# Performance work log

Measured on AMD Instinct MI355X. Metric: run time of the kernel, lower is better.

Reference implementation:

```python
import jax, jax.numpy as jnp
import numpy as np

N_NODES = 100000
N_EDGES = 1200000
IN_DIM, HIDDEN, OUT_DIM = 128, 64, 64


def setup_inputs() -> dict:
    key = jax.random.key(0)
    k1, k2, k3, k4 = jax.random.split(key, 4)
    x = jax.random.normal(k1, (N_NODES, IN_DIM), dtype=jnp.float32)
    edge_index = jax.random.randint(k2, (2, N_EDGES), 0, N_NODES, dtype=jnp.int64)
    # Glorot-style init for GCNConv linear weights (PyG uses glorot), zero bias.
    W1 = jax.random.normal(k3, (IN_DIM, HIDDEN), dtype=jnp.float32) * np.float32(np.sqrt(2.0 / (IN_DIM + HIDDEN)))
    b1 = jnp.zeros((HIDDEN,), dtype=jnp.float32)
    W2 = jax.random.normal(k4, (HIDDEN, OUT_DIM), dtype=jnp.float32) * np.float32(np.sqrt(2.0 / (HIDDEN + OUT_DIM)))
    b2 = jnp.zeros((OUT_DIM,), dtype=jnp.float32)
    return {"x": x, "edge_index": edge_index, "W1": W1, "b1": b1, "W2": W2, "b2": b2}


def _gcn_conv(h, src, dst, deg_inv_sqrt, W, b):
    # PyG GCNConv: out = scatter_add( norm * (h @ W)[src] -> dst ) + b
    n = h.shape[0]
    norm = deg_inv_sqrt[src] * deg_inv_sqrt[dst]            # [E+N]
    hw = h @ W                                              # [N, F_out]
    msg = hw[src] * norm[:, None]                           # [E+N, F_out] gather
    out = jnp.zeros((n, W.shape[1]), h.dtype).at[dst].add(msg)  # scatter-add
    return out + b


def reference(x, edge_index, W1, b1, W2, b2):
    n = x.shape[0]
    # Add self-loops (GCNConv default add_self_loops=True).
    loop = jnp.arange(n, dtype=edge_index.dtype)
    src = jnp.concatenate([edge_index[0], loop])  # source nodes
    dst = jnp.concatenate([edge_index[1], loop])  # target nodes (aggregation)
    # Symmetric normalization D^{-1/2} (A+I) D^{-1/2}; degree at targets.
    deg = jnp.zeros((n,), x.dtype).at[dst].add(jnp.ones((), x.dtype))
    deg_inv_sqrt = jnp.where(deg > 0, jax.lax.rsqrt(deg), 0.0)
    h = _gcn_conv(x, src, dst, deg_inv_sqrt, W1, b1)
    h = jax.nn.relu(h)
    h = _gcn_conv(h, src, dst, deg_inv_sqrt, W2, b2)
    h = jax.nn.relu(h)
    return h
```

## Files before the change

### kernel.cpp

```cpp
#include <hip/hip_runtime.h>
#include <hip/hip_fp16.h>
#include <cstdint>
#include <cstddef>

#define NN 100000
#define NE 1200000
#define NBKT 1563
#define CAP_B 1536
#define PBLK 256
#define PCHK ((NE + PBLK - 1) / PBLK)

typedef _Float16 f16x8 __attribute__((ext_vector_type(8)));
typedef float f32x4 __attribute__((ext_vector_type(4)));

__global__ void zero_kernel(int* __restrict__ cur, unsigned* __restrict__ ovfn) {
    int i = blockIdx.x * blockDim.x + threadIdx.x;
    if (i < NBKT) cur[i] = 0;
    if (i == NBKT) *ovfn = 0;
}

__global__ __launch_bounds__(256) void partition_hier(
    const int* __restrict__ ei, int* __restrict__ cur,
    unsigned* __restrict__ recs, unsigned* __restrict__ ovfn,
    uint2* __restrict__ ovf, int E) {
    __shared__ int hist[NBKT];
    __shared__ int base[NBKT];
    const int tid = threadIdx.x;
    for (int i = tid; i < NBKT; i += 256) hist[i] = 0;
    __syncthreads();
    const int lo = blockIdx.x * PCHK, hi = min(lo + PCHK, E);
    for (int e = lo + tid; e < hi; e += 256)
        atomicAdd(&hist[ei[E + e] >> 6], 1);
    __syncthreads();
    for (int i = tid; i < NBKT; i += 256) {
        int c = hist[i];
        base[i] = c ? atomicAdd(&cur[i], c) : 0;
        hist[i] = 0;
    }
    __syncthreads();
    for (int e = lo + tid; e < hi; e += 256) {
        int d = ei[E + e];
        int s = ei[e];
        int b = d >> 6;
        int lp = atomicAdd(&hist[b], 1);
        int pos = base[b] + lp;
        if (pos < CAP_B)
            recs[(size_t)b * CAP_B + pos] = ((unsigned)s << 6) | (unsigned)(d & 63);
        else {
            unsigned o = atomicAdd(ovfn, 1);
            if (o < 4096) ovf[o] = make_uint2((unsigned)s, (unsigned)d);
        }
    }
}

__global__ __launch_bounds__(256) void sort_bucket(
    const int* __restrict__ cur, unsigned* __restrict__ recs,
    const unsigned* __restrict__ ovfn, const uint2* __restrict__ ovf,
    float* __restrict__ dis, int* __restrict__ offn, int n) {
    __shared__ unsigned raw[CAP_B], srt[CAP_B];
    __shared__ int cnt[64], pfx[64], woff[64];
    const int b = blockIdx.x, tid = threadIdx.x;
    if (tid < 64) cnt[tid] = 0;
    const int c = min(cur[b], CAP_B);
    unsigned* slab = recs + (size_t)b * CAP_B;
    for (int i = tid; i < c; i += 256) raw[i] = slab[i];
    __syncthreads();
    for (int i = tid; i < c; i += 256) atomicAdd(&cnt[raw[i] & 63], 1);
    __syncthreads();
    if (tid < 64) pfx[tid] = cnt[tid];
    __syncthreads();
    for (int s = 1; s < 64; s <<= 1) {
        int v = (tid < 64 && tid >= s) ? pfx[tid - s] : 0;
        __syncthreads();
        if (tid < 64) pfx[tid] += v;
        __syncthreads();
    }
    if (tid < 64) woff[tid] = pfx[tid] - cnt[tid];
    __syncthreads();
    for (int i = tid; i < c; i += 256) {
        unsigned k = raw[i];
        int p = atomicAdd(&woff[k & 63], 1);
        srt[p] = k >> 6;
    }
    __syncthreads();
    for (int i = tid; i < c; i += 256) slab[i] = srt[i];
    if (tid < 64) {
        int g = b * 64 + tid;
        if (g < n) {
            int cc = cnt[tid];
            unsigned no = *ovfn;
            for (unsigned i = 0; i < no; i++)
                if ((int)ovf[i].y == g) cc++;
            dis[g] = rsqrtf((float)cc + 1.0f);
            offn[g] = pfx[tid] - cnt[tid];
        }
    }
}

template <bool HALF_OUT>
__global__ __launch_bounds__(256) void agg_bucket4(
    const int* __restrict__ cur, const unsigned* __restrict__ recs,
    const int* __restrict__ offn, const __half* __restrict__ hw,
    const float* __restrict__ dis, const float* __restrict__ bias,
    void* __restrict__ outv,
    const unsigned* __restrict__ ovfn, const uint2* __restrict__ ovf, int n) {
    __shared__ unsigned srec[CAP_B];
    __shared__ int soff[65];
    __shared__ float disD[64];
    const int b = blockIdx.x, tid = threadIdx.x;
    const int c = min(cur[b], CAP_B);
    const unsigned* slab = recs + (size_t)b * CAP_B;
    for (int i = tid; i < c; i += 256) srec[i] = slab[i];
    if (tid < 64) {
        int g = b * 64 + tid;
        disD[tid] = (g < n) ? dis[g] : 0.f;
        soff[tid] = (g < n) ? offn[g] : c;
    }
    if (tid == 0) soff[64] = c;
    __syncthreads();

    const uint2* hwq = (const uint2*)hw;
    const int slot = tid >> 4, sub = tid & 15;
    const unsigned no = *ovfn;
    const float4 bb = ((const float4*)bias)[sub];

#define LD1(q) { float2 g01 = __half22float2(*(__half2*)&(q).x); \
                 float2 g23 = __half22float2(*(__half2*)&(q).y); \
                 a0 += g01.x; a1 += g01.y; a2 += g23.x; a3 += g23.y; }

    for (int j = 0; j < 4; j++) {
        int nl = slot * 4 + j;
        int g = b * 64 + nl;
        if (g >= n) break;
        uint2 qs = hwq[(size_t)g * 16 + sub];
        float a0 = 0.f, a1 = 0.f, a2 = 0.f, a3 = 0.f;
        LD1(qs);

        int e = soff[nl], end = (nl < 63) ? soff[nl + 1] : soff[64];
        for (; e + 8 <= end; e += 8) {
            uint2 q0 = hwq[(size_t)srec[e + 0] * 16 + sub];
            uint2 q1 = hwq[(size_t)srec[e + 1] * 16 + sub];
            uint2 q2 = hwq[(size_t)srec[e + 2] * 16 + sub];
            uint2 q3 = hwq[(size_t)srec[e + 3] * 16 + sub];
            uint2 q4 = hwq[(size_t)srec[e + 4] * 16 + sub];
            uint2 q5 = hwq[(size_t)srec[e + 5] * 16 + sub];
            uint2 q6 = hwq[(size_t)srec[e + 6] * 16 + sub];
            uint2 q7 = hwq[(size_t)srec[e + 7] * 16 + sub];
            LD1(q0); LD1(q1); LD1(q2); LD1(q3);
            LD1(q4); LD1(q5); LD1(q6); LD1(q7);
        }
        for (; e + 4 <= end; e += 4) {
            uint2 q0 = hwq[(size_t)srec[e + 0] * 16 + sub];
            uint2 q1 = hwq[(size_t)srec[e + 1] * 16 + sub];
            uint2 q2 = hwq[(size_t)srec[e + 2] * 16 + sub];
            uint2 q3 = hwq[(size_t)srec[e + 3] * 16 + sub];
            LD1(q0); LD1(q1); LD1(q2); LD1(q3);
        }
        for (; e < end; e++) {
            uint2 q = hwq[(size_t)srec[e] * 16 + sub];
            LD1(q);
        }
        for (unsigned i = 0; i < no; i++) {
            uint2 o = ovf[i];
            if ((int)o.y == g) { uint2 q = hwq[(size_t)o.x * 16 + sub]; LD1(q); }
        }
        float di = disD[nl];
        float o0 = fmaf(di, a0, bb.x);
        float o1 = fmaf(di, a1, bb.y);
        float o2 = fmaf(di, a2, bb.z);
        float o3 = fmaf(di, a3, bb.w);
        o0 = o0 > 0.f ? o0 : 0.f;
        o1 = o1 > 0.f ? o1 : 0.f;
        o2 = o2 > 0.f ? o2 : 0.f;
        o3 = o3 > 0.f ? o3 : 0.f;
        if (HALF_OUT) {
            __half2 p01 = __floats2half2_rn(o0, o1);
            __half2 p23 = __floats2half2_rn(o2, o3);
            uint2 pk;
            pk.x = *(unsigned*)&p01;
            pk.y = *(unsigned*)&p23;
            ((uint2*)outv)[(size_t)g * 16 + sub] = pk;
        } else {
            float4 oo; oo.x = o0; oo.y = o1; oo.z = o2; oo.w = o3;
            ((float4*)outv)[(size_t)g * 16 + sub] = oo;
        }
    }
#undef LD1
}

template <int K>
__global__ __launch_bounds__(256) void gemm_mfma(const float* __restrict__ A,
                                                 const float* __restrict__ W,
                                                 const float* __restrict__ dis,
                                                 __half* __restrict__ C, int n) {
    constexpr int KB = K / 32;
    __shared__ f16x8 sAf[4 * KB * 64];
    __shared__ f16x8 sWf[4 * KB * 64];
    __shared__ float sdis[64];
    const int tid = threadIdx.x;
    const int row0 = blockIdx.x * 64;

    if (tid < 64) {
        int rw = row0 + tid;
        sdis[tid] = (rw < n) ? dis[rw] : 0.f;
    }

    _Float16* sAh = (_Float16*)sAf;
    const float4* A4 = (const float4*)A;
#pragma unroll
    for (int it = 0; it < K / 16; ++it) {
        int f = it * 256 + tid;
        int row = f / (K / 4);
        int kq = f % (K / 4);
        int k0 = kq * 4;
        float4 a;
        if (row0 + row < n) a = A4[(size_t)(row0 + row) * (K / 4) + kq];
        else { a.x = 0.f; a.y = 0.f; a.z = 0.f; a.w = 0.f; }
        int rt = row >> 4;
        int kb = k0 >> 5;
        int lane = (row & 15) | (((k0 >> 3) & 3) << 4);
        int base = ((rt * KB + kb) * 64 + lane) * 8 + (k0 & 7);
        sAh[base + 0] = (_Float16)a.x;
        sAh[base + 1] = (_Float16)a.y;
        sAh[base + 2] = (_Float16)a.z;
        sAh[base + 3] = (_Float16)a.w;
    }
    _Float16* sWh = (_Float16*)sWf;
    {
        int nn = tid & 63;
        int ct = nn >> 4;
        int lbase = nn & 15;
        for (int k = tid >> 6; k < K; k += 4) {
            float w = W[(size_t)k * 64 + nn];
            int kb = k >> 5;
            int lane = lbase | (((k >> 3) & 3) << 4);
            sWh[((ct * KB + kb) * 64 + lane) * 8 + (k & 7)] = (_Float16)w;
        }
    }
    __syncthreads();

    const int wv = tid >> 6;
    const int lane = tid & 63;
    f32x4 acc[4];
#pragma unroll
    for (int rt = 0; rt < 4; ++rt) acc[rt] = (f32x4){0.f, 0.f, 0.f, 0.f};

#pragma unroll
    for (int kb = 0; kb < KB; ++kb) {
        f16x8 bf = sWf[(wv * KB + kb) * 64 + lane];
#pragma unroll
        for (int rt = 0; rt < 4; ++rt) {
            f16x8 af = sAf[(rt * KB + kb) * 64 + lane];
            acc[rt] = __builtin_amdgcn_mfma_f32_16x16x32_f16(af, bf, acc[rt], 0, 0, 0);
        }
    }

    int col = wv * 16 + (lane & 15);
    int rbase = (lane >> 4) * 4;
#pragma unroll
    for (int rt = 0; rt < 4; ++rt) {
#pragma unroll
        for (int r = 0; r < 4; ++r) {
            int row = row0 + rt * 16 + rbase + r;
            if (row < n)
                C[(size_t)row * 64 + col] = __float2half(acc[rt][r] * sdis[rt * 16 + rbase + r]);
        }
    }
}

__global__ __launch_bounds__(256) void gemm_mfma_h(const __half* __restrict__ A,
                                                   const float* __restrict__ W,
                                                   const float* __restrict__ dis,
                                                   __half* __restrict__ C, int n) {
    constexpr int K = 64, KB = 2;
    __shared__ f16x8 sAf[4 * KB * 64];
    __shared__ f16x8 sWf[4 * KB * 64];
    __shared__ float sdis[64];
    const int tid = threadIdx.x;
    const int row0 = blockIdx.x * 64;

    if (tid < 64) {
        int rw = row0 + tid;
        sdis[tid] = (rw < n) ? dis[rw] : 0.f;
    }

    _Float16* sAh = (_Float16*)sAf;
    const uint2* A2 = (const uint2*)A;
#pragma unroll
    for (int it = 0; it < 4; ++it) {
        int f = it * 256 + tid;
        int row = f >> 4;
        int kq = f & 15;
        int k0 = kq * 4;
        uint2 a;
        if (row0 + row < n) a = A2[(size_t)(row0 + row) * 16 + kq];
        else { a.x = 0u; a.y = 0u; }
        _Float16* ap = (_Float16*)&a;
        int rt = row >> 4;
        int kb = k0 >> 5;
        int lane = (row & 15) | (((k0 >> 3) & 3) << 4);
        int base = ((rt * KB + kb) * 64 + lane) * 8 + (k0 & 7);
        sAh[base + 0] = ap[0];
        sAh[base + 1] = ap[1];
        sAh[base + 2] = ap[2];
        sAh[base + 3] = ap[3];
    }
    _Float16* sWh = (_Float16*)sWf;
    {
        int nn = tid & 63;
        int ct = nn >> 4;
        int lbase = nn & 15;
        for (int k = tid >> 6; k < K; k += 4) {
            float w = W[(size_t)k * 64 + nn];
            int kb = k >> 5;
            int lane = lbase | (((k >> 3) & 3) << 4);
            sWh[((ct * KB + kb) * 64 + lane) * 8 + (k & 7)] = (_Float16)w;
        }
    }
    __syncthreads();

    const int wv = tid >> 6;
    const int lane = tid & 63;
    f32x4 acc[4];
#pragma unroll
    for (int rt = 0; rt < 4; ++rt) acc[rt] = (f32x4){0.f, 0.f, 0.f, 0.f};

#pragma unroll
    for (int kb = 0; kb < KB; ++kb) {
        f16x8 bf = sWf[(wv * KB + kb) * 64 + lane];
#pragma unroll
        for (int rt = 0; rt < 4; ++rt) {
            f16x8 af = sAf[(rt * KB + kb) * 64 + lane];
            acc[rt] = __builtin_amdgcn_mfma_f32_16x16x32_f16(af, bf, acc[rt], 0, 0, 0);
        }
    }

    int col = wv * 16 + (lane & 15);
    int rbase = (lane >> 4) * 4;
#pragma unroll
    for (int rt = 0; rt < 4; ++rt) {
#pragma unroll
        for (int r = 0; r < 4; ++r) {
            int row = row0 + rt * 16 + rbase + r;
            if (row < n)
                C[(size_t)row * 64 + col] = __float2half(acc[rt][r] * sdis[rt * 16 + rbase + r]);
        }
    }
}

__global__ void fill_kernel(float* __restrict__ p, float v, int n) {
    int i = blockIdx.x * blockDim.x + threadIdx.x;
    if (i < n) p[i] = v;
}
__global__ void degree_kernel(const int* __restrict__ ei, float* __restrict__ deg, int E) {
    int stride = gridDim.x * blockDim.x;
    for (int e = blockIdx.x * blockDim.x + threadIdx.x; e < E; e += stride)
        atomicAdd(&deg[ei[E + e]], 1.0f);
}
__global__ void rsqrt_kernel(float* __restrict__ deg, int n) {
    int i = blockIdx.x * blockDim.x + threadIdx.x;
    if (i < n) deg[i] = rsqrtf(deg[i]);
}
template <int K>
__global__ __launch_bounds__(256) void gemm_tile(const float* __restrict__ A,
                                                 const float* __restrict__ W,
                                                 float* __restrict__ C, int n) {
    __shared__ float sA[64 * K];
    __shared__ float sW[K * 64];
    const int tid = threadIdx.x;
    const int row0 = blockIdx.x * 64;
    const int rows = min(64, n - row0);
    const float4* W4 = (const float4*)W;
    float4* sW4 = (float4*)sW;
    for (int i = tid; i < K * 16; i += 256) sW4[i] = W4[i];
    const float4* A4 = (const float4*)(A + (size_t)row0 * K);
    float4* sA4 = (float4*)sA;
    const int nElem = rows * (K / 4);
    for (int i = tid; i < nElem; i += 256) sA4[i] = A4[i];
    __syncthreads();
    const int col = tid & 63;
    const int ty  = tid >> 6;
    float acc[16];
#pragma unroll
    for (int r = 0; r < 16; r++) acc[r] = 0.f;
    for (int k = 0; k < K; k += 4) {
        float w0 = sW[(k + 0) * 64 + col];
        float w1 = sW[(k + 1) * 64 + col];
        float w2 = sW[(k + 2) * 64 + col];
        float w3 = sW[(k + 3) * 64 + col];
#pragma unroll
        for (int r = 0; r < 16; r++) {
            const float4 a = *(const float4*)&sA[(ty + 4 * r) * K + k];
            acc[r] = fmaf(a.x, w0, acc[r]);
            acc[r] = fmaf(a.y, w1, acc[r]);
            acc[r] = fmaf(a.z, w2, acc[r]);
            acc[r] = fmaf(a.w, w3, acc[r]);
        }
    }
#pragma unroll
    for (int r = 0; r < 16; r++) {
        int row = ty + 4 * r;
        if (row < rows) C[(size_t)(row0 + row) * 64 + col] = acc[r];
    }
}
__global__ void scatter_kernel(const int* __restrict__ ei, const float* __restrict__ hw,
                               const float* __restrict__ dis, float* __restrict__ agg, int E) {
    int gtid = blockIdx.x * blockDim.x + threadIdx.x;
    int wave = gtid >> 6, lane = threadIdx.x & 63;
    int nwaves = (gridDim.x * blockDim.x) >> 6;
    for (int e = wave; e < E; e += nwaves) {
        int s = ei[e], d = ei[E + e];
        float v = hw[(size_t)s * 64 + lane] * dis[s] * dis[d];
        atomicAdd(&agg[(size_t)d * 64 + lane], v);
    }
}
__global__ void finalize_kernel(float* __restrict__ agg, const float* __restrict__ hw,
                                const float* __restrict__ dis, const float* __restrict__ b, int n) {
    int i = blockIdx.x * blockDim.x + threadIdx.x;
    if (i < n * 64) {
        int node = i >> 6, col = i & 63;
        float di = dis[node];
        float v = agg[i] + hw[i] * di * di + b[col];
        agg[i] = v > 0.0f ? v : 0.0f;
    }
}

extern "C" void kernel_launch(void* const* d_in, const int* in_sizes, int n_in,
                              void* d_out, int out_size, void* d_ws, size_t ws_size,
                              hipStream_t stream) {
    const float* x  = (const float*)d_in[0];
    const int*   ei = (const int*)d_in[1];
    const float* W1 = (const float*)d_in[2];
    const float* b1 = (const float*)d_in[3];
    const float* W2 = (const float*)d_in[4];
    const float* b2 = (const float*)d_in[5];
    float* out = (float*)d_out;

    const int N = NN, E = NE;
    char* ws = (char*)d_ws;
    const int gemmGrid = (N + 63) / 64;

    if (ws_size >= 38200000u) {
        float*    dis  = (float*)ws;
        int*      cur  = (int*)(ws + (1u << 19));
        unsigned* ovfn = (unsigned*)(ws + 589824u);
        uint2*    ovf  = (uint2*)(ws + 593920u);
        int*      offn = (int*)(ws + 655360u);
        unsigned* recs = (unsigned*)(ws + 1572864u);
        __half*   hwa  = (__half*)(ws + 11534336u);
        __half*   hvb  = (__half*)(ws + 25165824u);

        zero_kernel<<<(NBKT + 256) / 256, 256, 0, stream>>>(cur, ovfn);
        partition_hier<<<PBLK, 256, 0, stream>>>(ei, cur, recs, ovfn, ovf, E);
        sort_bucket<<<NBKT, 256, 0, stream>>>(cur, recs, ovfn, ovf, dis, offn, N);

        gemm_mfma<128><<<gemmGrid, 256, 0, stream>>>(x, W1, dis, hwa, N);
        agg_bucket4<true><<<NBKT, 256, 0, stream>>>(cur, recs, offn, hwa, dis, b1, hvb, ovfn, ovf, N);
        gemm_mfma_h<<<gemmGrid, 256, 0, stream>>>(hvb, W2, dis, hwa, N);
        agg_bucket4<false><<<NBKT, 256, 0, stream>>>(cur, recs, offn, hwa, dis, b2, out, ovfn, ovf, N);
    } else {
        float* dis  = (float*)ws;
        float* bufA = (float*)(ws + (1 << 19));
        const size_t featBytes = (size_t)N * 64 * sizeof(float);

        fill_kernel<<<(N + 255) / 256, 256, 0, stream>>>(dis, 1.0f, N);
        degree_kernel<<<2048, 256, 0, stream>>>(ei, dis, E);
        rsqrt_kernel<<<(N + 255) / 256, 256, 0, stream>>>(dis, N);

        gemm_tile<128><<<gemmGrid, 256, 0, stream>>>(x, W1, bufA, N);
        hipMemsetAsync(out, 0, featBytes, stream);
        scatter_kernel<<<2048, 256, 0, stream>>>(ei, bufA, dis, out, E);
        finalize_kernel<<<(N * 64 + 255) / 256, 256, 0, stream>>>(out, bufA, dis, b1, N);

        gemm_tile<64><<<gemmGrid, 256, 0, stream>>>(out, W2, bufA, N);
        hipMemsetAsync(out, 0, featBytes, stream);
        scatter_kernel<<<2048, 256, 0, stream>>>(ei, bufA, dis, out, E);
        finalize_kernel<<<(N * 64 + 255) / 256, 256, 0, stream>>>(out, bufA, dis, b2, N);
    }
}
```

Measured before the change: 123.7 us.

## Fuse layer-1 aggregation with layer-2 MFMA GEMM and widen partition blocks

Layer-1 aggregation output is now kept in a swizzled shared-memory fp16 tile, and the layer-2 GEMM runs on it inside the same block using MFMA. This removes one kernel launch and the global write and read of the intermediate hidden features. The partition kernel now uses 1024 threads per block instead of 256, and the 4-wide tail loop in aggregation is dropped. The fused kernel uses more shared memory per block, which may lower occupancy in the gather-bound aggregation phase.

```diff
diff --git a/kernel.cpp b/kernel.cpp
--- a/kernel.cpp
+++ b/kernel.cpp
@@ -19,26 +19,26 @@
     if (i == NBKT) *ovfn = 0;
 }
 
-__global__ __launch_bounds__(256) void partition_hier(
+__global__ __launch_bounds__(1024) void partition_hier(
     const int* __restrict__ ei, int* __restrict__ cur,
     unsigned* __restrict__ recs, unsigned* __restrict__ ovfn,
     uint2* __restrict__ ovf, int E) {
     __shared__ int hist[NBKT];
     __shared__ int base[NBKT];
     const int tid = threadIdx.x;
-    for (int i = tid; i < NBKT; i += 256) hist[i] = 0;
+    for (int i = tid; i < NBKT; i += 1024) hist[i] = 0;
     __syncthreads();
     const int lo = blockIdx.x * PCHK, hi = min(lo + PCHK, E);
-    for (int e = lo + tid; e < hi; e += 256)
+    for (int e = lo + tid; e < hi; e += 1024)
         atomicAdd(&hist[ei[E + e] >> 6], 1);
     __syncthreads();
-    for (int i = tid; i < NBKT; i += 256) {
+    for (int i = tid; i < NBKT; i += 1024) {
         int c = hist[i];
         base[i] = c ? atomicAdd(&cur[i], c) : 0;
         hist[i] = 0;
     }
     __syncthreads();
-    for (int e = lo + tid; e < hi; e += 256) {
+    for (int e = lo + tid; e < hi; e += 1024) {
         int d = ei[E + e];
         int s = ei[e];
         int b = d >> 6;
@@ -97,12 +97,132 @@
     }
 }
 
-template <bool HALF_OUT>
+#define LD1(q) { float2 g01 = __half22float2(*(__half2*)&(q).x); \
+                 float2 g23 = __half22float2(*(__half2*)&(q).y); \
+                 a0 += g01.x; a1 += g01.y; a2 += g23.x; a3 += g23.y; }
+
+__global__ __launch_bounds__(256) void agg_gemm_fused(
+    const int* __restrict__ cur, const unsigned* __restrict__ recs,
+    const int* __restrict__ offn, const __half* __restrict__ hw,
+    const float* __restrict__ dis, const float* __restrict__ bias,
+    const float* __restrict__ W2, __half* __restrict__ outHwa,
+    const unsigned* __restrict__ ovfn, const uint2* __restrict__ ovf, int n) {
+    __shared__ unsigned srec[CAP_B];
+    __shared__ int soff[65];
+    __shared__ float disD[64];
+    __shared__ _Float16 htile[64 * 64];
+    __shared__ f16x8 sWf[4 * 2 * 64];
+    const int b = blockIdx.x, tid = threadIdx.x;
+    const int c = min(cur[b], CAP_B);
+    const unsigned* slab = recs + (size_t)b * CAP_B;
+    for (int i = tid; i < c; i += 256) srec[i] = slab[i];
+    if (tid < 64) {
+        int g = b * 64 + tid;
+        disD[tid] = (g < n) ? dis[g] : 0.f;
+        soff[tid] = (g < n) ? offn[g] : c;
+    }
+    if (tid == 0) soff[64] = c;
+    {
+        _Float16* sWh = (_Float16*)sWf;
+        int nn = tid & 63, ct = nn >> 4, lbase = nn & 15;
+        for (int k = tid >> 6; k < 64; k += 4) {
+            float w = W2[(size_t)k * 64 + nn];
+            int kb = k >> 5;
+            int lane = lbase | (((k >> 3) & 3) << 4);
+            sWh[((ct * 2 + kb) * 64 + lane) * 8 + (k & 7)] = (_Float16)w;
+        }
+    }
+    __syncthreads();
+
+    const uint2* hwq = (const uint2*)hw;
+    const int slot = tid >> 4, sub = tid & 15;
+    const unsigned no = *ovfn;
+    const float4 bb = ((const float4*)bias)[sub];
+
+    for (int j = 0; j < 4; j++) {
+        int nl = slot * 4 + j;
+        int g = b * 64 + nl;
+        float o0 = 0.f, o1 = 0.f, o2 = 0.f, o3 = 0.f;
+        if (g < n) {
+            uint2 qs = hwq[(size_t)g * 16 + sub];
+            float a0 = 0.f, a1 = 0.f, a2 = 0.f, a3 = 0.f;
+            LD1(qs);
+            int e = soff[nl], end = soff[nl + 1];
+            for (; e + 8 <= end; e += 8) {
+                uint2 q0 = hwq[(size_t)srec[e + 0] * 16 + sub];
+                uint2 q1 = hwq[(size_t)srec[e + 1] * 16 + sub];
+                uint2 q2 = hwq[(size_t)srec[e + 2] * 16 + sub];
+                uint2 q3 = hwq[(size_t)srec[e + 3] * 16 + sub];
+                uint2 q4 = hwq[(size_t)srec[e + 4] * 16 + sub];
+                uint2 q5 = hwq[(size_t)srec[e + 5] * 16 + sub];
+                uint2 q6 = hwq[(size_t)srec[e + 6] * 16 + sub];
+                uint2 q7 = hwq[(size_t)srec[e + 7] * 16 + sub];
+                LD1(q0); LD1(q1); LD1(q2); LD1(q3);
+                LD1(q4); LD1(q5); LD1(q6); LD1(q7);
+            }
+            for (; e < end; e++) {
+                uint2 q = hwq[(size_t)srec[e] * 16 + sub];
+                LD1(q);
+            }
+            for (unsigned i = 0; i < no; i++) {
+                uint2 o = ovf[i];
+                if ((int)o.y == g) { uint2 q = hwq[(size_t)o.x * 16 + sub]; LD1(q); }
+            }
+            float di = disD[nl];
+            o0 = fmaf(di, a0, bb.x);
+            o1 = fmaf(di, a1, bb.y);
+            o2 = fmaf(di, a2, bb.z);
+            o3 = fmaf(di, a3, bb.w);
+            o0 = o0 > 0.f ? o0 : 0.f;
+            o1 = o1 > 0.f ? o1 : 0.f;
+            o2 = o2 > 0.f ? o2 : 0.f;
+            o3 = o3 > 0.f ? o3 : 0.f;
+        }
+        __half2 p01 = __floats2half2_rn(o0, o1);
+        __half2 p23 = __floats2half2_rn(o2, o3);
+        uint2 pk;
+        pk.x = *(unsigned*)&p01;
+        pk.y = *(unsigned*)&p23;
+        int phys = (sub >> 1) ^ (nl & 7);
+        *(uint2*)&htile[nl * 64 + phys * 8 + (sub & 1) * 4] = pk;
+    }
+    __syncthreads();
+
+    const int wv = tid >> 6;
+    const int lane = tid & 63;
+    f32x4 acc[4];
+#pragma unroll
+    for (int rt = 0; rt < 4; ++rt) acc[rt] = (f32x4){0.f, 0.f, 0.f, 0.f};
+#pragma unroll
+    for (int kb = 0; kb < 2; ++kb) {
+        f16x8 bf = sWf[(wv * 2 + kb) * 64 + lane];
+#pragma unroll
+        for (int rt = 0; rt < 4; ++rt) {
+            int row = rt * 16 + (lane & 15);
+            int g0 = kb * 4 + (lane >> 4);
+            f16x8 af = *(f16x8*)&htile[row * 64 + ((g0 ^ (row & 7)) << 3)];
+            acc[rt] = __builtin_amdgcn_mfma_f32_16x16x32_f16(af, bf, acc[rt], 0, 0, 0);
+        }
+    }
+    int col = wv * 16 + (lane & 15);
+    int rbase = (lane >> 4) * 4;
+#pragma unroll
+    for (int rt = 0; rt < 4; ++rt) {
+#pragma unroll
+        for (int r = 0; r < 4; ++r) {
+            int rowl = rt * 16 + rbase + r;
+            int row = b * 64 + rowl;
+            if (row < n)
+                outHwa[(size_t)row * 64 + col] = __float2half(acc[rt][r] * disD[rowl]);
+        }
+    }
+}
+
 __global__ __launch_bounds__(256) void agg_bucket4(
     const int* __restrict__ cur, const unsigned* __restrict__ recs,
     const int* __restrict__ offn, const __half* __restrict__ hw,
     const float* __restrict__ dis, const float* __restrict__ bias,
-    void* __restrict__ outv,
+    float* __restrict__ out,
     const unsigned* __restrict__ ovfn, const uint2* __restrict__ ovf, int n) {
     __shared__ unsigned srec[CAP_B];
     __shared__ int soff[65];
@@ -124,10 +244,6 @@
     const unsigned no = *ovfn;
     const float4 bb = ((const float4*)bias)[sub];
 
-#define LD1(q) { float2 g01 = __half22float2(*(__half2*)&(q).x); \
-                 float2 g23 = __half22float2(*(__half2*)&(q).y); \
-                 a0 += g01.x; a1 += g01.y; a2 += g23.x; a3 += g23.y; }
-
     for (int j = 0; j < 4; j++) {
         int nl = slot * 4 + j;
         int g = b * 64 + nl;
@@ -135,8 +251,7 @@
         uint2 qs = hwq[(size_t)g * 16 + sub];
         float a0 = 0.f, a1 = 0.f, a2 = 0.f, a3 = 0.f;
         LD1(qs);
-
-        int e = soff[nl], end = (nl < 63) ? soff[nl + 1] : soff[64];
+        int e = soff[nl], end = soff[nl + 1];
         for (; e + 8 <= end; e += 8) {
             uint2 q0 = hwq[(size_t)srec[e + 0] * 16 + sub];
             uint2 q1 = hwq[(size_t)srec[e + 1] * 16 + sub];
@@ -149,13 +264,6 @@
             LD1(q0); LD1(q1); LD1(q2); LD1(q3);
             LD1(q4); LD1(q5); LD1(q6); LD1(q7);
         }
-        for (; e + 4 <= end; e += 4) {
-            uint2 q0 = hwq[(size_t)srec[e + 0] * 16 + sub];
-            uint2 q1 = hwq[(size_t)srec[e + 1] * 16 + sub];
-            uint2 q2 = hwq[(size_t)srec[e + 2] * 16 + sub];
-            uint2 q3 = hwq[(size_t)srec[e + 3] * 16 + sub];
-            LD1(q0); LD1(q1); LD1(q2); LD1(q3);
-        }
         for (; e < end; e++) {
             uint2 q = hwq[(size_t)srec[e] * 16 + sub];
             LD1(q);
@@ -165,27 +273,17 @@
             if ((int)o.y == g) { uint2 q = hwq[(size_t)o.x * 16 + sub]; LD1(q); }
         }
         float di = disD[nl];
-        float o0 = fmaf(di, a0, bb.x);
-        float o1 = fmaf(di, a1, bb.y);
-        float o2 = fmaf(di, a2, bb.z);
-        float o3 = fmaf(di, a3, bb.w);
-        o0 = o0 > 0.f ? o0 : 0.f;
-        o1 = o1 > 0.f ? o1 : 0.f;
-        o2 = o2 > 0.f ? o2 : 0.f;
-        o3 = o3 > 0.f ? o3 : 0.f;
-        if (HALF_OUT) {
-            __half2 p01 = __floats2half2_rn(o0, o1);
-            __half2 p23 = __floats2half2_rn(o2, o3);
-            uint2 pk;
-            pk.x = *(unsigned*)&p01;
-            pk.y = *(unsigned*)&p23;
-            ((uint2*)outv)[(size_t)g * 16 + sub] = pk;
-        } else {
-            float4 oo; oo.x = o0; oo.y = o1; oo.z = o2; oo.w = o3;
-            ((float4*)outv)[(size_t)g * 16 + sub] = oo;
-        }
-    }
-#undef LD1
+        float4 oo;
+        oo.x = fmaf(di, a0, bb.x);
+        oo.y = fmaf(di, a1, bb.y);
+        oo.z = fmaf(di, a2, bb.z);
+        oo.w = fmaf(di, a3, bb.w);
+        oo.x = oo.x > 0.f ? oo.x : 0.f;
+        oo.y = oo.y > 0.f ? oo.y : 0.f;
+        oo.z = oo.z > 0.f ? oo.z : 0.f;
+        oo.w = oo.w > 0.f ? oo.w : 0.f;
+        ((float4*)out)[(size_t)g * 16 + sub] = oo;
+    }
 }
 
 template <int K>
@@ -268,86 +366,6 @@
     }
 }
 
-__global__ __launch_bounds__(256) void gemm_mfma_h(const __half* __restrict__ A,
-                                                   const float* __restrict__ W,
-                                                   const float* __restrict__ dis,
-                                                   __half* __restrict__ C, int n) {
-    constexpr int K = 64, KB = 2;
-    __shared__ f16x8 sAf[4 * KB * 64];
-    __shared__ f16x8 sWf[4 * KB * 64];
-    __shared__ float sdis[64];
-    const int tid = threadIdx.x;
-    const int row0 = blockIdx.x * 64;
-
-    if (tid < 64) {
-        int rw = row0 + tid;
-        sdis[tid] = (rw < n) ? dis[rw] : 0.f;
-    }
-
-    _Float16* sAh = (_Float16*)sAf;
-    const uint2* A2 = (const uint2*)A;
-#pragma unroll
-    for (int it = 0; it < 4; ++it) {
-        int f = it * 256 + tid;
-        int row = f >> 4;
-        int kq = f & 15;
-        int k0 = kq * 4;
-        uint2 a;
-        if (row0 + row < n) a = A2[(size_t)(row0 + row) * 16 + kq];
-        else { a.x = 0u; a.y = 0u; }
-        _Float16* ap = (_Float16*)&a;
-        int rt = row >> 4;
-        int kb = k0 >> 5;
-        int lane = (row & 15) | (((k0 >> 3) & 3) << 4);
-        int base = ((rt * KB + kb) * 64 + lane) * 8 + (k0 & 7);
-        sAh[base + 0] = ap[0];
-        sAh[base + 1] = ap[1];
-        sAh[base + 2] = ap[2];
-        sAh[base + 3] = ap[3];
-    }
-    _Float16* sWh = (_Float16*)sWf;
-    {
-        int nn = tid & 63;
-        int ct = nn >> 4;
-        int lbase = nn & 15;
-        for (int k = tid >> 6; k < K; k += 4) {
-            float w = W[(size_t)k * 64 + nn];
-            int kb = k >> 5;
-            int lane = lbase | (((k >> 3) & 3) << 4);
-            sWh[((ct * KB + kb) * 64 + lane) * 8 + (k & 7)] = (_Float16)w;
-        }
-    }
-    __syncthreads();
-
-    const int wv = tid >> 6;
-    const int lane = tid & 63;
-    f32x4 acc[4];
-#pragma unroll
-    for (int rt = 0; rt < 4; ++rt) acc[rt] = (f32x4){0.f, 0.f, 0.f, 0.f};
-
-#pragma unroll
-    for (int kb = 0; kb < KB; ++kb) {
-        f16x8 bf = sWf[(wv * KB + kb) * 64 + lane];
-#pragma unroll
-        for (int rt = 0; rt < 4; ++rt) {
-            f16x8 af = sAf[(rt * KB + kb) * 64 + lane];
-            acc[rt] = __builtin_amdgcn_mfma_f32_16x16x32_f16(af, bf, acc[rt], 0, 0, 0);
-        }
-    }
-
-    int col = wv * 16 + (lane & 15);
-    int rbase = (lane >> 4) * 4;
-#pragma unroll
-    for (int rt = 0; rt < 4; ++rt) {
-#pragma unroll
-        for (int r = 0; r < 4; ++r) {
-            int row = row0 + rt * 16 + rbase + r;
-            if (row < n)
-                C[(size_t)row * 64 + col] = __float2half(acc[rt][r] * sdis[rt * 16 + rbase + r]);
-        }
-    }
-}
-
 __global__ void fill_kernel(float* __restrict__ p, float v, int n) {
     int i = blockIdx.x * blockDim.x + threadIdx.x;
     if (i < n) p[i] = v;
@@ -451,13 +469,13 @@
         __half*   hvb  = (__half*)(ws + 25165824u);
 
         zero_kernel<<<(NBKT + 256) / 256, 256, 0, stream>>>(cur, ovfn);
-        partition_hier<<<PBLK, 256, 0, stream>>>(ei, cur, recs, ovfn, ovf, E);
+        partition_hier<<<PBLK, 1024, 0, stream>>>(ei, cur, recs, ovfn, ovf, E);
         sort_bucket<<<NBKT, 256, 0, stream>>>(cur, recs, ovfn, ovf, dis, offn, N);
 
         gemm_mfma<128><<<gemmGrid, 256, 0, stream>>>(x, W1, dis, hwa, N);
-        agg_bucket4<true><<<NBKT, 256, 0, stream>>>(cur, recs, offn, hwa, dis, b1, hvb, ovfn, ovf, N);
-        gemm_mfma_h<<<gemmGrid, 256, 0, stream>>>(hvb, W2, dis, hwa, N);
-        agg_bucket4<false><<<NBKT, 256, 0, stream>>>(cur, recs, offn, hwa, dis, b2, out, ovfn, ovf, N);
+        agg_gemm_fused<<<NBKT, 256, 0, stream>>>(cur, recs, offn, hwa, dis, b1, W2, hvb,
+                                                 ovfn, ovf, N);
+        agg_bucket4<<<NBKT, 256, 0, stream>>>(cur, recs, offn, hvb, dis, b2, out, ovfn, ovf, N);
     } else {
         float* dis  = (float*)ws;
         float* bufA = (float*)(ws + (1 << 19));
```

Measured after the change: 119.4 us. 1.04x faster.

## Store hidden features as column strips and aggregate one strip per block

Applied to the files above, without the earlier changes.

The GEMM outputs now write the fp16 hidden features as four 16-column strips instead of one 64-wide row layout. The second GEMM reads its input in that strip layout. Aggregation is split into 8 small blocks per bucket, one for each strip and half-bucket, each reading source indices straight from global memory instead of staging them in LDS. The aim is more parallelism, smaller per-gather working sets and better cache behaviour for the random gathers. In exchange, edge lists are re-read once per strip and each gather is only 32 bytes. The partition kernel also moves to 1024-thread blocks.

```diff
diff --git a/kernel.cpp b/kernel.cpp
--- a/kernel.cpp
+++ b/kernel.cpp
@@ -9,6 +9,8 @@
 #define CAP_B 1536
 #define PBLK 256
 #define PCHK ((NE + PBLK - 1) / PBLK)
+#define SSTR2 (NBKT * 64 * 4)
+#define SSTRH (NBKT * 64 * 16)
 
 typedef _Float16 f16x8 __attribute__((ext_vector_type(8)));
 typedef float f32x4 __attribute__((ext_vector_type(4)));
@@ -19,26 +21,26 @@
     if (i == NBKT) *ovfn = 0;
 }
 
-__global__ __launch_bounds__(256) void partition_hier(
+__global__ __launch_bounds__(1024) void partition_hier(
     const int* __restrict__ ei, int* __restrict__ cur,
     unsigned* __restrict__ recs, unsigned* __restrict__ ovfn,
     uint2* __restrict__ ovf, int E) {
     __shared__ int hist[NBKT];
     __shared__ int base[NBKT];
     const int tid = threadIdx.x;
-    for (int i = tid; i < NBKT; i += 256) hist[i] = 0;
+    for (int i = tid; i < NBKT; i += 1024) hist[i] = 0;
     __syncthreads();
     const int lo = blockIdx.x * PCHK, hi = min(lo + PCHK, E);
-    for (int e = lo + tid; e < hi; e += 256)
+    for (int e = lo + tid; e < hi; e += 1024)
         atomicAdd(&hist[ei[E + e] >> 6], 1);
     __syncthreads();
-    for (int i = tid; i < NBKT; i += 256) {
+    for (int i = tid; i < NBKT; i += 1024) {
         int c = hist[i];
         base[i] = c ? atomicAdd(&cur[i], c) : 0;
         hist[i] = 0;
     }
     __syncthreads();
-    for (int e = lo + tid; e < hi; e += 256) {
+    for (int e = lo + tid; e < hi; e += 1024) {
         int d = ei[E + e];
         int s = ei[e];
         int b = d >> 6;
@@ -97,95 +99,93 @@
     }
 }
 
+#define LD1(q) { float2 g01 = __half22float2(*(__half2*)&(q).x); \
+                 float2 g23 = __half22float2(*(__half2*)&(q).y); \
+                 a0 += g01.x; a1 += g01.y; a2 += g23.x; a3 += g23.y; }
+
 template <bool HALF_OUT>
-__global__ __launch_bounds__(256) void agg_bucket4(
+__global__ __launch_bounds__(128) void agg_strip(
     const int* __restrict__ cur, const unsigned* __restrict__ recs,
     const int* __restrict__ offn, const __half* __restrict__ hw,
     const float* __restrict__ dis, const float* __restrict__ bias,
     void* __restrict__ outv,
     const unsigned* __restrict__ ovfn, const uint2* __restrict__ ovf, int n) {
-    __shared__ unsigned srec[CAP_B];
-    __shared__ int soff[65];
-    __shared__ float disD[64];
-    const int b = blockIdx.x, tid = threadIdx.x;
+    __shared__ int soff[33];
+    __shared__ float sdis[32];
+    const int bid = blockIdx.x, tid = threadIdx.x;
+    const int b = bid >> 3;
+    const int q = bid & 3;
+    const int h = (bid >> 2) & 1;
     const int c = min(cur[b], CAP_B);
+
+    if (tid < 33) {
+        int g2 = b * 64 + h * 32 + tid;
+        soff[tid] = ((h == 1 && tid == 32) || g2 >= n) ? c : offn[g2];
+    }
+    if (tid < 32) {
+        int g2 = b * 64 + h * 32 + tid;
+        sdis[tid] = (g2 < n) ? dis[g2] : 0.f;
+    }
+    __syncthreads();
+
+    const int nl = tid >> 2;
+    const int sub = tid & 3;
+    const int g = b * 64 + h * 32 + nl;
+    if (g >= n) return;
+
+    const uint2* hq = (const uint2*)hw + (size_t)q * SSTR2;
     const unsigned* slab = recs + (size_t)b * CAP_B;
-    for (int i = tid; i < c; i += 256) srec[i] = slab[i];
-    if (tid < 64) {
-        int g = b * 64 + tid;
-        disD[tid] = (g < n) ? dis[g] : 0.f;
-        soff[tid] = (g < n) ? offn[g] : c;
-    }
-    if (tid == 0) soff[64] = c;
-    __syncthreads();
-
-    const uint2* hwq = (const uint2*)hw;
-    const int slot = tid >> 4, sub = tid & 15;
-    const unsigned no = *ovfn;
-    const float4 bb = ((const float4*)bias)[sub];
-
-#define LD1(q) { float2 g01 = __half22float2(*(__half2*)&(q).x); \
-                 float2 g23 = __half22float2(*(__half2*)&(q).y); \
-                 a0 += g01.x; a1 += g01.y; a2 += g23.x; a3 += g23.y; }
-
-    for (int j = 0; j < 4; j++) {
-        int nl = slot * 4 + j;
-        int g = b * 64 + nl;
-        if (g >= n) break;
-        uint2 qs = hwq[(size_t)g * 16 + sub];
-        float a0 = 0.f, a1 = 0.f, a2 = 0.f, a3 = 0.f;
-        LD1(qs);
-
-        int e = soff[nl], end = (nl < 63) ? soff[nl + 1] : soff[64];
-        for (; e + 8 <= end; e += 8) {
-            uint2 q0 = hwq[(size_t)srec[e + 0] * 16 + sub];
-            uint2 q1 = hwq[(size_t)srec[e + 1] * 16 + sub];
-            uint2 q2 = hwq[(size_t)srec[e + 2] * 16 + sub];
-            uint2 q3 = hwq[(size_t)srec[e + 3] * 16 + sub];
-            uint2 q4 = hwq[(size_t)srec[e + 4] * 16 + sub];
-            uint2 q5 = hwq[(size_t)srec[e + 5] * 16 + sub];
-            uint2 q6 = hwq[(size_t)srec[e + 6] * 16 + sub];
-            uint2 q7 = hwq[(size_t)srec[e + 7] * 16 + sub];
-            LD1(q0); LD1(q1); LD1(q2); LD1(q3);
-            LD1(q4); LD1(q5); LD1(q6); LD1(q7);
-        }
-        for (; e + 4 <= end; e += 4) {
-            uint2 q0 = hwq[(size_t)srec[e + 0] * 16 + sub];
-            uint2 q1 = hwq[(size_t)srec[e + 1] * 16 + sub];
-            uint2 q2 = hwq[(size_t)srec[e + 2] * 16 + sub];
-            uint2 q3 = hwq[(size_t)srec[e + 3] * 16 + sub];
-            LD1(q0); LD1(q1); LD1(q2); LD1(q3);
-        }
-        for (; e < end; e++) {
-            uint2 q = hwq[(size_t)srec[e] * 16 + sub];
-            LD1(q);
-        }
-        for (unsigned i = 0; i < no; i++) {
-            uint2 o = ovf[i];
-            if ((int)o.y == g) { uint2 q = hwq[(size_t)o.x * 16 + sub]; LD1(q); }
-        }
-        float di = disD[nl];
-        float o0 = fmaf(di, a0, bb.x);
-        float o1 = fmaf(di, a1, bb.y);
-        float o2 = fmaf(di, a2, bb.z);
-        float o3 = fmaf(di, a3, bb.w);
-        o0 = o0 > 0.f ? o0 : 0.f;
-        o1 = o1 > 0.f ? o1 : 0.f;
-        o2 = o2 > 0.f ? o2 : 0.f;
-        o3 = o3 > 0.f ? o3 : 0.f;
-        if (HALF_OUT) {
-            __half2 p01 = __floats2half2_rn(o0, o1);
-            __half2 p23 = __floats2half2_rn(o2, o3);
-            uint2 pk;
-            pk.x = *(unsigned*)&p01;
-            pk.y = *(unsigned*)&p23;
-            ((uint2*)outv)[(size_t)g * 16 + sub] = pk;
-        } else {
-            float4 oo; oo.x = o0; oo.y = o1; oo.z = o2; oo.w = o3;
-            ((float4*)outv)[(size_t)g * 16 + sub] = oo;
-        }
-    }
-#undef LD1
+
+    uint2 qs = hq[(size_t)g * 4 + sub];
+    float a0 = 0.f, a1 = 0.f, a2 = 0.f, a3 = 0.f;
+    LD1(qs);
+
+    int e = soff[nl], end = soff[nl + 1];
+    for (; e + 8 <= end; e += 8) {
+        unsigned s0 = slab[e + 0], s1 = slab[e + 1], s2 = slab[e + 2], s3 = slab[e + 3];
+        unsigned s4 = slab[e + 4], s5 = slab[e + 5], s6 = slab[e + 6], s7 = slab[e + 7];
+        uint2 q0 = hq[(size_t)s0 * 4 + sub];
+        uint2 q1 = hq[(size_t)s1 * 4 + sub];
+        uint2 q2 = hq[(size_t)s2 * 4 + sub];
+        uint2 q3 = hq[(size_t)s3 * 4 + sub];
+        uint2 q4 = hq[(size_t)s4 * 4 + sub];
+        uint2 q5 = hq[(size_t)s5 * 4 + sub];
+        uint2 q6 = hq[(size_t)s6 * 4 + sub];
+        uint2 q7 = hq[(size_t)s7 * 4 + sub];
+        LD1(q0); LD1(q1); LD1(q2); LD1(q3);
+        LD1(q4); LD1(q5); LD1(q6); LD1(q7);
+    }
+    for (; e < end; e++) {
+        uint2 qq = hq[(size_t)slab[e] * 4 + sub];
+        LD1(qq);
+    }
+    unsigned no = *ovfn;
+    for (unsigned i = 0; i < no; i++) {
+        uint2 o = ovf[i];
+        if ((int)o.y == g) { uint2 qq = hq[(size_t)o.x * 4 + sub]; LD1(qq); }
+    }
+
+    float di = sdis[nl];
+    const float4 bb = ((const float4*)bias)[q * 4 + sub];
+    float o0 = fmaf(di, a0, bb.x);
+    float o1 = fmaf(di, a1, bb.y);
+    float o2 = fmaf(di, a2, bb.z);
+    float o3 = fmaf(di, a3, bb.w);
+    o0 = o0 > 0.f ? o0 : 0.f;
+    o1 = o1 > 0.f ? o1 : 0.f;
+    o2 = o2 > 0.f ? o2 : 0.f;
+    o3 = o3 > 0.f ? o3 : 0.f;
+    if (HALF_OUT) {
+        __half2 p01 = __floats2half2_rn(o0, o1);
+        __half2 p23 = __floats2half2_rn(o2, o3);
+        uint2 pk;
+        pk.x = *(unsigned*)&p01;
+        pk.y = *(unsigned*)&p23;
+        ((uint2*)outv)[(size_t)q * SSTR2 + (size_t)g * 4 + sub] = pk;
+    } else {
+        float4 oo; oo.x = o0; oo.y = o1; oo.z = o2; oo.w = o3;
+        ((float4*)outv)[(size_t)g * 16 + q * 4 + sub] = oo;
+    }
 }
 
 template <int K>
@@ -255,7 +255,7 @@
         }
     }
 
-    int col = wv * 16 + (lane & 15);
+    int col16 = lane & 15;
     int rbase = (lane >> 4) * 4;
 #pragma unroll
     for (int rt = 0; rt < 4; ++rt) {
@@ -263,7 +263,8 @@
         for (int r = 0; r < 4; ++r) {
             int row = row0 + rt * 16 + rbase + r;
             if (row < n)
-                C[(size_t)row * 64 + col] = __float2half(acc[rt][r] * sdis[rt * 16 + rbase + r]);
+                C[(size_t)wv * SSTRH + (size_t)row * 16 + col16] =
+                    __float2half(acc[rt][r] * sdis[rt * 16 + rbase + r]);
         }
     }
 }
@@ -292,8 +293,9 @@
         int row = f >> 4;
         int kq = f & 15;
         int k0 = kq * 4;
+        int q = kq >> 2;
         uint2 a;
-        if (row0 + row < n) a = A2[(size_t)(row0 + row) * 16 + kq];
+        if (row0 + row < n) a = A2[(size_t)q * SSTR2 + (size_t)(row0 + row) * 4 + (kq & 3)];
         else { a.x = 0u; a.y = 0u; }
         _Float16* ap = (_Float16*)&a;
         int rt = row >> 4;
@@ -335,7 +337,7 @@
         }
     }
 
-    int col = wv * 16 + (lane & 15);
+    int col16 = lane & 15;
     int rbase = (lane >> 4) * 4;
 #pragma unroll
     for (int rt = 0; rt < 4; ++rt) {
@@ -343,7 +345,8 @@
         for (int r = 0; r < 4; ++r) {
             int row = row0 + rt * 16 + rbase + r;
             if (row < n)
-                C[(size_t)row * 64 + col] = __float2half(acc[rt][r] * sdis[rt * 16 + rbase + r]);
+                C[(size_t)wv * SSTRH + (size_t)row * 16 + col16] =
+                    __float2half(acc[rt][r] * sdis[rt * 16 + rbase + r]);
         }
     }
 }
@@ -448,16 +451,18 @@
         int*      offn = (int*)(ws + 655360u);
         unsigned* recs = (unsigned*)(ws + 1572864u);
         __half*   hwa  = (__half*)(ws + 11534336u);
-        __half*   hvb  = (__half*)(ws + 25165824u);
+        __half*   hvb  = (__half*)(ws + 24641536u);
 
         zero_kernel<<<(NBKT + 256) / 256, 256, 0, stream>>>(cur, ovfn);
-        partition_hier<<<PBLK, 256, 0, stream>>>(ei, cur, recs, ovfn, ovf, E);
+        partition_hier<<<PBLK, 1024, 0, stream>>>(ei, cur, recs, ovfn, ovf, E);
         sort_bucket<<<NBKT, 256, 0, stream>>>(cur, recs, ovfn, ovf, dis, offn, N);
 
         gemm_mfma<128><<<gemmGrid, 256, 0, stream>>>(x, W1, dis, hwa, N);
-        agg_bucket4<true><<<NBKT, 256, 0, stream>>>(cur, recs, offn, hwa, dis, b1, hvb, ovfn, ovf, N);
+        agg_strip<true><<<NBKT * 8, 128, 0, stream>>>(cur, recs, offn, hwa, dis, b1, hvb,
+                                                      ovfn, ovf, N);
         gemm_mfma_h<<<gemmGrid, 256, 0, stream>>>(hvb, W2, dis, hwa, N);
-        agg_bucket4<false><<<NBKT, 256, 0, stream>>>(cur, recs, offn, hwa, dis, b2, out, ovfn, ovf, N);
+        agg_strip<false><<<NBKT * 8, 128, 0, stream>>>(cur, recs, offn, hwa, dis, b2, out,
+                                                       ovfn, ovf, N);
     } else {
         float* dis  = (float*)ws;
         float* bufA = (float*)(ws + (1 << 19));
```

New measurement: 148.3 us. 1.2x slower.
